# Performance work log

Measured on AMD Instinct MI355X. Metric: run time of the kernel, lower is better.

The kernel has to match this reference:

```python
import jax, jax.numpy as jnp
import numpy as np

ROPE_BASE = 10000.0
NEG = -1e9

def _rope_tables(N, head_dim, dtype):
    # freq buffer: angles[pos, i] = pos / base^(2i/head_dim), i over half dim
    inv = 1.0 / (ROPE_BASE ** (jnp.arange(0, head_dim, 2, dtype=jnp.float32) / head_dim))
    ang = jnp.arange(N, dtype=jnp.float32)[:, None] * inv[None, :]  # (N, hd/2)
    return jnp.cos(ang).astype(dtype), jnp.sin(ang).astype(dtype)

def _apply_rope(t, cos, sin):
    # t: (B, h, N, hd); rotate-half style
    hd = t.shape[-1]
    t1, t2 = t[..., : hd // 2], t[..., hd // 2 :]
    c = cos[None, None]  # (1,1,N,hd/2)
    s = sin[None, None]
    return jnp.concatenate([t1 * c - t2 * s, t1 * s + t2 * c], axis=-1)


def setup_inputs() -> dict:
    key = jax.random.key(0)
    B, N, D, h = 2, 2048, 2048, 16
    ks = jax.random.split(key, 5)
    x = jax.random.normal(ks[0], (B, N, D), dtype=jnp.float32)
    Wqkv = jax.random.normal(ks[1], (3 * D, D), dtype=jnp.float32) * 0.02
    Wproj = jax.random.normal(ks[2], (D, D), dtype=jnp.float32) * 0.02
    bproj = jax.random.normal(ks[3], (D,), dtype=jnp.float32) * 0.02
    L = jax.random.randint(ks[4], (B,), 1, N + 1, dtype=jnp.int32)
    return {"x": x, "Wqkv": Wqkv, "Wproj": Wproj, "bproj": bproj, "L": L, "n_heads": 16}


def reference(x, Wqkv, Wproj, bproj, L, n_heads):
    B, N, D = x.shape
    hd = D // n_heads
    scale = 1.0 / jnp.sqrt(jnp.asarray(hd, dtype=x.dtype))

    # fused QKV projection (no bias)
    qkv = jnp.einsum('bnd,ed->bne', x, Wqkv)  # (B, N, 3D)
    q, k, v = jnp.split(qkv, 3, axis=-1)
    # (B, N, h*hd) -> (B, h, N, hd)
    def heads(t):
        return t.reshape(B, N, n_heads, hd).transpose(0, 2, 1, 3)
    q, k, v = heads(q), heads(k), heads(v)

    cos, sin = _rope_tables(N, hd, x.dtype)
    q = _apply_rope(q, cos, sin)
    k = _apply_rope(k, cos, sin)

    # causal + key-padding mask (pos < L valid)
    pos = jnp.arange(N)
    causal = pos[:, None] >= pos[None, :]                    # (N, N)
    key_valid = pos[None, :] < L[:, None]                    # (B, N)
    mask = causal[None, None] & key_valid[:, None, None, :]  # (B,1,N,N)

    scores = jnp.einsum('bhqd,bhkd->bhqk', q, k) * scale
    scores = jnp.where(mask, scores, NEG)
    attn = jax.nn.softmax(scores, axis=-1)
    out = jnp.einsum('bhqk,bhkd->bhqd', attn, v)             # (B,h,N,hd)
    out = out.transpose(0, 2, 1, 3).reshape(B, N, D)
    return jnp.einsum('bnd,ed->bne', out, Wproj) + bproj
```

## Files before the change

kernel.cpp:

```cpp
#include <hip/hip_runtime.h>
#include <hip/hip_bf16.h>


typedef unsigned short u16;
typedef short bf16x8 __attribute__((ext_vector_type(8)));
typedef unsigned short u16x8 __attribute__((ext_vector_type(8)));
typedef float f32x4 __attribute__((ext_vector_type(4)));

#define MFMA16(a, b, c) __builtin_amdgcn_mfma_f32_16x16x32_bf16((a), (b), (c), 0, 0, 0)

__device__ __forceinline__ float b2f(u16 u) { return __uint_as_float(((unsigned)u) << 16); }
__device__ __forceinline__ u16 f2b(float f) {
    unsigned x = __float_as_uint(f);
    return (u16)((x + 0x7fffu + ((x >> 16) & 1u)) >> 16);
}
__device__ __forceinline__ void gload16(const u16* g, u16* lds) {
    __builtin_amdgcn_global_load_lds((__attribute__((address_space(1))) void*)g,
                                     (__attribute__((address_space(3))) void*)lds,
                                     16, 0, 0);
}

__global__ __launch_bounds__(256) void cvt_bf16(const float* __restrict__ in,
                                                u16* __restrict__ out) {
    size_t i = (size_t)blockIdx.x * 256 + threadIdx.x;
    float4 a = ((const float4*)in)[2 * i];
    float4 b = ((const float4*)in)[2 * i + 1];
    u16x8 o;
    o[0] = f2b(a.x); o[1] = f2b(a.y); o[2] = f2b(a.z); o[3] = f2b(a.w);
    o[4] = f2b(b.x); o[5] = f2b(b.y); o[6] = f2b(b.z); o[7] = f2b(b.w);
    ((u16x8*)out)[i] = o;
}

__global__ __launch_bounds__(256) void rope_tables_k(float* __restrict__ cosT,
                                                     float* __restrict__ sinT) {
    int idx = blockIdx.x * 256 + threadIdx.x;
    int n = idx >> 6, i = idx & 63;
    float inv = powf(10000.0f, -(float)(2 * i) / 128.0f);
    float ang = (float)n * inv;
    cosT[idx] = cosf(ang);
    sinT[idx] = sinf(ang);
}

template <int OUTF32>
__global__ __launch_bounds__(256, 2) void gemm_nt(const u16* __restrict__ A,
                                                  const u16* __restrict__ B,
                                                  void* __restrict__ Cv,
                                                  const float* __restrict__ bias,
                                                  int M, int Ncols, int K) {
    __shared__ u16 As[128 * 64];
    __shared__ u16 Bs[128 * 64];
    const int tx = threadIdx.x;
    const int w = tx >> 6, l = tx & 63;
    const int fr = l & 15, fg = l >> 4;
    const int wr = w >> 1, wc = w & 1;
    const long row0 = (long)blockIdx.x * 128;
    const long col0 = (long)blockIdx.y * 128;
    f32x4 acc[4][4] = {};
    const int nk = K >> 6;
    int rs[4], ss[4];
#pragma unroll
    for (int i = 0; i < 4; ++i) {
        int c = i * 256 + tx;
        rs[i] = c >> 3;
        ss[i] = (c & 7) ^ ((c >> 3) & 7);
    }
    for (int kt = 0; kt < nk; ++kt) {
        const long k0 = (long)kt << 6;
        __syncthreads();
#pragma unroll
        for (int i = 0; i < 4; ++i)
            gload16(A + (row0 + rs[i]) * K + k0 + ss[i] * 8, &As[(i * 256 + w * 64) * 8]);
#pragma unroll
        for (int i = 0; i < 4; ++i)
            gload16(B + (col0 + rs[i]) * K + k0 + ss[i] * 8, &Bs[(i * 256 + w * 64) * 8]);
        __syncthreads();
#pragma unroll
        for (int kk = 0; kk < 2; ++kk) {
            bf16x8 af[4], bfv[4];
#pragma unroll
            for (int m = 0; m < 4; ++m) {
                int r = wr * 64 + m * 16 + fr;
                af[m] = *(const bf16x8*)&As[r * 64 + (((kk * 4 + fg) ^ (r & 7)) << 3)];
            }
#pragma unroll
            for (int n = 0; n < 4; ++n) {
                int r = wc * 64 + n * 16 + fr;
                bfv[n] = *(const bf16x8*)&Bs[r * 64 + (((kk * 4 + fg) ^ (r & 7)) << 3)];
            }
#pragma unroll
            for (int m = 0; m < 4; ++m)
#pragma unroll
                for (int n = 0; n < 4; ++n) acc[m][n] = MFMA16(af[m], bfv[n], acc[m][n]);
        }
    }
#pragma unroll
    for (int m = 0; m < 4; ++m) {
#pragma unroll
        for (int n = 0; n < 4; ++n) {
#pragma unroll
            for (int r = 0; r < 4; ++r) {
                long row = row0 + wr * 64 + m * 16 + fg * 4 + r;
                long col = col0 + wc * 64 + n * 16 + fr;
                float v = acc[m][n][r];
                if (OUTF32) {
                    ((float*)Cv)[row * Ncols + col] = v + bias[col];
                } else {
                    ((u16*)Cv)[row * Ncols + col] = f2b(v);
                }
            }
        }
    }
}

__global__ __launch_bounds__(256) void rope_transpose_k(
    const u16* __restrict__ qkv, const float* __restrict__ cosT,
    const float* __restrict__ sinT, u16* __restrict__ Q, u16* __restrict__ Ko,
    u16* __restrict__ VT) {
    const int bh = blockIdx.y, b = bh >> 4, h = bh & 15;
    const int n0 = blockIdx.x << 7;
    const int tx = threadIdx.x;
    __shared__ u16 vbuf[128][136];
    const float SCALE = 0.08838834764831844f;
#pragma unroll
    for (int pass = 0; pass < 4; ++pass) {
        const int rr = pass * 32 + (tx >> 3);
        const int p = tx & 7;
        const int n = n0 + rr;
        const u16* src = qkv + ((size_t)(b * 2048 + n)) * 6144 + h * 128;
        float c[8], s[8];
#pragma unroll
        for (int j = 0; j < 8; ++j) {
            c[j] = cosT[n * 64 + p * 8 + j];
            s[j] = sinT[n * 64 + p * 8 + j];
        }
        {
            u16x8 t1 = *(const u16x8*)&src[p * 8];
            u16x8 t2 = *(const u16x8*)&src[64 + p * 8];
            u16x8 o1, o2;
#pragma unroll
            for (int j = 0; j < 8; ++j) {
                float a = b2f(t1[j]), bb = b2f(t2[j]);
                o1[j] = f2b((a * c[j] - bb * s[j]) * SCALE);
                o2[j] = f2b((a * s[j] + bb * c[j]) * SCALE);
            }
            u16* dst = Q + ((size_t)bh * 2048 + n) * 128;
            *(u16x8*)&dst[p * 8] = o1;
            *(u16x8*)&dst[64 + p * 8] = o2;
        }
        {
            u16x8 t1 = *(const u16x8*)&src[2048 + p * 8];
            u16x8 t2 = *(const u16x8*)&src[2048 + 64 + p * 8];
            u16x8 o1, o2;
#pragma unroll
            for (int j = 0; j < 8; ++j) {
                float a = b2f(t1[j]), bb = b2f(t2[j]);
                o1[j] = f2b(a * c[j] - bb * s[j]);
                o2[j] = f2b(a * s[j] + bb * c[j]);
            }
            u16* dst = Ko + ((size_t)bh * 2048 + n) * 128;
            *(u16x8*)&dst[p * 8] = o1;
            *(u16x8*)&dst[64 + p * 8] = o2;
        }
    }
#pragma unroll
    for (int i = 0; i < 8; ++i) {
        int cid = i * 256 + tx;
        int rr = cid >> 4, cc = cid & 15;
        *(u16x8*)&vbuf[rr][cc * 8] =
            *(const u16x8*)&qkv[((size_t)(b * 2048 + n0 + rr)) * 6144 + 4096 + h * 128 + cc * 8];
    }
    __syncthreads();
#pragma unroll
    for (int i = 0; i < 8; ++i) {
        int cid = i * 256 + tx;
        int j = cid >> 4, nc = cid & 15;
        u16x8 o;
#pragma unroll
        for (int e = 0; e < 8; ++e) o[e] = vbuf[nc * 8 + e][j];
        *(u16x8*)&VT[((size_t)bh * 128 + j) * 2048 + n0 + nc * 8] = o;
    }
}

__global__ __launch_bounds__(256, 2) void attn_k(const u16* __restrict__ Q,
                                                 const u16* __restrict__ K,
                                                 const u16* __restrict__ VT,
                                                 u16* __restrict__ O,
                                                 const int* __restrict__ L) {
    const int bh = blockIdx.y, b = bh >> 4, h = bh & 15;
    const int qx = blockIdx.x;
    const int qb0 = qx << 6, qb1 = (31 - qx) << 6;
    const int tx = threadIdx.x;
    const int w = tx >> 6, l = tx & 63;
    const int fr = l & 15, fg = l >> 4;
    const int Lb = L[b];
    __shared__ u16 Ks[64 * 128];
    __shared__ u16 Vs[128 * 64];
    __shared__ u16 Ps[4][16 * 72];
    const u16* Qh = Q + (size_t)bh * 2048 * 128;
    const u16* Kh = K + (size_t)bh * 2048 * 128;
    const u16* Vh = VT + (size_t)bh * 128 * 2048;
    bf16x8 aq0[4], aq1[4];
#pragma unroll
    for (int kc = 0; kc < 4; ++kc) {
        aq0[kc] = *(const bf16x8*)&Qh[(size_t)(qb0 + w * 16 + fr) * 128 + kc * 32 + fg * 8];
        aq1[kc] = *(const bf16x8*)&Qh[(size_t)(qb1 + w * 16 + fr) * 128 + kc * 32 + fg * 8];
    }
    f32x4 accO0[8] = {}, accO1[8] = {};
    float mr0[4] = {-1e30f, -1e30f, -1e30f, -1e30f};
    float mr1[4] = {-1e30f, -1e30f, -1e30f, -1e30f};
    float sr0[4] = {0.f, 0.f, 0.f, 0.f};
    float sr1[4] = {0.f, 0.f, 0.f, 0.f};
    const int kmax = min(qb1 + 63, Lb - 1);
    const int nkt = (kmax >> 6) + 1;

    auto do_strip = [&](const bf16x8 (&aqs)[4], float (&mr)[4], float (&sr)[4],
                        f32x4 (&aO)[8], int qgb, int kt0) {
        f32x4 accS[4];
#pragma unroll
        for (int st = 0; st < 4; ++st) {
            f32x4 z = {0.f, 0.f, 0.f, 0.f};
            accS[st] = z;
            int key = st * 16 + fr;
#pragma unroll
            for (int kc = 0; kc < 4; ++kc) {
                bf16x8 bk = *(const bf16x8*)&Ks[key * 128 + (((kc * 4 + fg) ^ (key & 7)) << 3)];
                accS[st] = MFMA16(aqs[kc], bk, accS[st]);
            }
        }
        float sv[4][4];
#pragma unroll
        for (int st = 0; st < 4; ++st)
#pragma unroll
            for (int r = 0; r < 4; ++r) {
                int key = kt0 + st * 16 + fr;
                int qg = qgb + fg * 4 + r;
                sv[st][r] = (key <= qg && key < Lb) ? accS[st][r] : -1e30f;
            }
        float alpha[4], pr[4][4];
#pragma unroll
        for (int r = 0; r < 4; ++r) {
            float lm = fmaxf(fmaxf(sv[0][r], sv[1][r]), fmaxf(sv[2][r], sv[3][r]));
            lm = fmaxf(lm, __shfl_xor(lm, 1));
            lm = fmaxf(lm, __shfl_xor(lm, 2));
            lm = fmaxf(lm, __shfl_xor(lm, 4));
            lm = fmaxf(lm, __shfl_xor(lm, 8));
            float mn = fmaxf(mr[r], lm);
            alpha[r] = exp2f((mr[r] - mn) * 1.44269504f);
            float ls = 0.f;
#pragma unroll
            for (int st = 0; st < 4; ++st) {
                float p = exp2f((sv[st][r] - mn) * 1.44269504f);
                pr[st][r] = p;
                ls += p;
            }
            ls += __shfl_xor(ls, 1);
            ls += __shfl_xor(ls, 2);
            ls += __shfl_xor(ls, 4);
            ls += __shfl_xor(ls, 8);
            sr[r] = sr[r] * alpha[r] + ls;
            mr[r] = mn;
        }
#pragma unroll
        for (int n = 0; n < 8; ++n)
#pragma unroll
            for (int r = 0; r < 4; ++r) aO[n][r] *= alpha[r];
#pragma unroll
        for (int st = 0; st < 4; ++st)
#pragma unroll
            for (int r = 0; r < 4; ++r)
                Ps[w][(fg * 4 + r) * 72 + st * 16 + fr] = f2b(pr[st][r]);
#pragma unroll
        for (int ks = 0; ks < 2; ++ks) {
            bf16x8 ap = *(const bf16x8*)&Ps[w][fr * 72 + ks * 32 + fg * 8];
#pragma unroll
            for (int n = 0; n < 8; ++n) {
                int d = n * 16 + fr;
                bf16x8 bv = *(const bf16x8*)&Vs[d * 64 + (((ks * 4 + fg) ^ (d & 7)) << 3)];
                aO[n] = MFMA16(ap, bv, aO[n]);
            }
        }
    };

    for (int kt = 0; kt < nkt; ++kt) {
        const int kt0 = kt << 6;
        __syncthreads();
#pragma unroll
        for (int i = 0; i < 4; ++i) {
            int c = i * 256 + tx;
            int row = c >> 4, cp = c & 15;
            gload16(Kh + (size_t)(kt0 + row) * 128 + ((cp ^ (row & 7)) << 3),
                    &Ks[(i * 256 + w * 64) * 8]);
        }
#pragma unroll
        for (int i = 0; i < 4; ++i) {
            int c = i * 256 + tx;
            int row = c >> 3, cp = c & 7;
            gload16(Vh + (size_t)row * 2048 + kt0 + ((cp ^ (row & 7)) << 3),
                    &Vs[(i * 256 + w * 64) * 8]);
        }
        __syncthreads();
        if (kt <= qx)
            do_strip(aq0, mr0, sr0, accO0, qb0 + w * 16, kt0);
        do_strip(aq1, mr1, sr1, accO1, qb1 + w * 16, kt0);
    }
    float inv0[4], inv1[4];
#pragma unroll
    for (int r = 0; r < 4; ++r) {
        inv0[r] = 1.0f / sr0[r];
        inv1[r] = 1.0f / sr1[r];
    }
#pragma unroll
    for (int n = 0; n < 8; ++n)
#pragma unroll
        for (int r = 0; r < 4; ++r) {
            int d = n * 16 + fr;
            int q0 = qb0 + w * 16 + fg * 4 + r;
            int q1 = qb1 + w * 16 + fg * 4 + r;
            O[((size_t)(b * 2048 + q0)) * 2048 + h * 128 + d] = f2b(accO0[n][r] * inv0[r]);
            O[((size_t)(b * 2048 + q1)) * 2048 + h * 128 + d] = f2b(accO1[n][r] * inv1[r]);
        }
}

extern "C" void kernel_launch(void* const* d_in, const int* in_sizes, int n_in,
                              void* d_out, int out_size, void* d_ws, size_t ws_size,
                              hipStream_t stream) {
    const float* x = (const float*)d_in[0];
    const float* Wqkv = (const float*)d_in[1];
    const float* Wproj = (const float*)d_in[2];
    const float* bproj = (const float*)d_in[3];
    const int* L = (const int*)d_in[4];
    float* out = (float*)d_out;

    char* p = (char*)d_ws;
    u16* xbf = (u16*)(p + 0);
    u16* wqkvbf = (u16*)(p + 16777216);
    u16* wprojbf = (u16*)(p + 41943040);
    u16* qkv = (u16*)(p + 50331648);
    u16* Kb = (u16*)(p + 100663296);
    u16* VTb = (u16*)(p + 117440512);
    float* cosT = (float*)(p + 134217728);
    float* sinT = (float*)(p + 134742016);
    u16* Ob = xbf;
    u16* Qb = wqkvbf;

    cvt_bf16<<<4096, 256, 0, stream>>>(x, xbf);
    cvt_bf16<<<6144, 256, 0, stream>>>(Wqkv, wqkvbf);
    cvt_bf16<<<2048, 256, 0, stream>>>(Wproj, wprojbf);
    rope_tables_k<<<512, 256, 0, stream>>>(cosT, sinT);
    gemm_nt<0><<<dim3(32, 48), 256, 0, stream>>>(xbf, wqkvbf, qkv, nullptr, 4096, 6144, 2048);
    rope_transpose_k<<<dim3(16, 32), 256, 0, stream>>>(qkv, cosT, sinT, Qb, Kb, VTb);
    attn_k<<<dim3(16, 32), 256, 0, stream>>>(Qb, Kb, VTb, Ob, L);
    gemm_nt<1><<<dim3(32, 16), 256, 0, stream>>>(Ob, wprojbf, out, bproj, 4096, 2048, 2048);
}
```

Measured before the change: 261.2 us.

## Double-buffer K/V tiles in attention and share K fragment reads across strips

K and V shared-memory tiles become double-buffered. The next tile's global-to-LDS loads are issued right after the per-iteration barrier, so they overlap the MFMA and softmax work on the current tile, and one barrier per iteration replaces two. The QK^T loop for both query strips is also merged so each K fragment read from LDS feeds two MFMAs. The cost is doubled LDS for K/V (about 73KB per block, which still allows two blocks per CU on this target) and higher register pressure from holding two score accumulator sets at once.

```diff
diff --git a/kernel.cpp b/kernel.cpp
--- a/kernel.cpp
+++ b/kernel.cpp
@@ -193,8 +193,8 @@
     const int w = tx >> 6, l = tx & 63;
     const int fr = l & 15, fg = l >> 4;
     const int Lb = L[b];
-    __shared__ u16 Ks[64 * 128];
-    __shared__ u16 Vs[128 * 64];
+    __shared__ u16 Ks[2][64 * 128];
+    __shared__ u16 Vs[2][128 * 64];
     __shared__ u16 Ps[4][16 * 72];
     const u16* Qh = Q + (size_t)bh * 2048 * 128;
     const u16* Kh = K + (size_t)bh * 2048 * 128;
@@ -213,20 +213,25 @@
     const int kmax = min(qb1 + 63, Lb - 1);
     const int nkt = (kmax >> 6) + 1;
 
-    auto do_strip = [&](const bf16x8 (&aqs)[4], float (&mr)[4], float (&sr)[4],
-                        f32x4 (&aO)[8], int qgb, int kt0) {
-        f32x4 accS[4];
-#pragma unroll
-        for (int st = 0; st < 4; ++st) {
-            f32x4 z = {0.f, 0.f, 0.f, 0.f};
-            accS[st] = z;
-            int key = st * 16 + fr;
-#pragma unroll
-            for (int kc = 0; kc < 4; ++kc) {
-                bf16x8 bk = *(const bf16x8*)&Ks[key * 128 + (((kc * 4 + fg) ^ (key & 7)) << 3)];
-                accS[st] = MFMA16(aqs[kc], bk, accS[st]);
-            }
-        }
+    auto stage_tile = [&](int kt0, int buf) {
+#pragma unroll
+        for (int i = 0; i < 4; ++i) {
+            int c = i * 256 + tx;
+            int row = c >> 4, cp = c & 15;
+            gload16(Kh + (size_t)(kt0 + row) * 128 + ((cp ^ (row & 7)) << 3),
+                    &Ks[buf][(i * 256 + w * 64) * 8]);
+        }
+#pragma unroll
+        for (int i = 0; i < 4; ++i) {
+            int c = i * 256 + tx;
+            int row = c >> 3, cp = c & 7;
+            gload16(Vh + (size_t)row * 2048 + kt0 + ((cp ^ (row & 7)) << 3),
+                    &Vs[buf][(i * 256 + w * 64) * 8]);
+        }
+    };
+
+    auto finish_strip = [&](f32x4 (&accS)[4], float (&mr)[4], float (&sr)[4],
+                            f32x4 (&aO)[8], int qgb, int kt0, const u16* Vsb) {
         float sv[4][4];
 #pragma unroll
         for (int st = 0; st < 4; ++st)
@@ -275,33 +280,53 @@
 #pragma unroll
             for (int n = 0; n < 8; ++n) {
                 int d = n * 16 + fr;
-                bf16x8 bv = *(const bf16x8*)&Vs[d * 64 + (((ks * 4 + fg) ^ (d & 7)) << 3)];
+                bf16x8 bv = *(const bf16x8*)&Vsb[d * 64 + (((ks * 4 + fg) ^ (d & 7)) << 3)];
                 aO[n] = MFMA16(ap, bv, aO[n]);
             }
         }
     };
 
+    stage_tile(0, 0);
+    int cur = 0;
     for (int kt = 0; kt < nkt; ++kt) {
         const int kt0 = kt << 6;
         __syncthreads();
-#pragma unroll
-        for (int i = 0; i < 4; ++i) {
-            int c = i * 256 + tx;
-            int row = c >> 4, cp = c & 15;
-            gload16(Kh + (size_t)(kt0 + row) * 128 + ((cp ^ (row & 7)) << 3),
-                    &Ks[(i * 256 + w * 64) * 8]);
-        }
-#pragma unroll
-        for (int i = 0; i < 4; ++i) {
-            int c = i * 256 + tx;
-            int row = c >> 3, cp = c & 7;
-            gload16(Vh + (size_t)row * 2048 + kt0 + ((cp ^ (row & 7)) << 3),
-                    &Vs[(i * 256 + w * 64) * 8]);
-        }
-        __syncthreads();
-        if (kt <= qx)
-            do_strip(aq0, mr0, sr0, accO0, qb0 + w * 16, kt0);
-        do_strip(aq1, mr1, sr1, accO1, qb1 + w * 16, kt0);
+        if (kt + 1 < nkt) stage_tile((kt + 1) << 6, cur ^ 1);
+        const u16* Ksb = Ks[cur];
+        const u16* Vsb = Vs[cur];
+        f32x4 s0[4], s1[4];
+        if (kt <= qx) {
+#pragma unroll
+            for (int st = 0; st < 4; ++st) {
+                f32x4 z = {0.f, 0.f, 0.f, 0.f};
+                s0[st] = z; s1[st] = z;
+                int key = st * 16 + fr;
+#pragma unroll
+                for (int kc = 0; kc < 4; ++kc) {
+                    bf16x8 bk =
+                        *(const bf16x8*)&Ksb[key * 128 + (((kc * 4 + fg) ^ (key & 7)) << 3)];
+                    s0[st] = MFMA16(aq0[kc], bk, s0[st]);
+                    s1[st] = MFMA16(aq1[kc], bk, s1[st]);
+                }
+            }
+            finish_strip(s0, mr0, sr0, accO0, qb0 + w * 16, kt0, Vsb);
+            finish_strip(s1, mr1, sr1, accO1, qb1 + w * 16, kt0, Vsb);
+        } else {
+#pragma unroll
+            for (int st = 0; st < 4; ++st) {
+                f32x4 z = {0.f, 0.f, 0.f, 0.f};
+                s1[st] = z;
+                int key = st * 16 + fr;
+#pragma unroll
+                for (int kc = 0; kc < 4; ++kc) {
+                    bf16x8 bk =
+                        *(const bf16x8*)&Ksb[key * 128 + (((kc * 4 + fg) ^ (key & 7)) << 3)];
+                    s1[st] = MFMA16(aq1[kc], bk, s1[st]);
+                }
+            }
+            finish_strip(s1, mr1, sr1, accO1, qb1 + w * 16, kt0, Vsb);
+        }
+        cur ^= 1;
     }
     float inv0[4], inv1[4];
 #pragma unroll
```

Result: slower. 352.7 us (+35.0%).
